# Kernel optimization log

Hardware: AMD Instinct MI355X
Metric: run time of the kernel (lower is better)

Reference implementation:

```python
import jax, jax.numpy as jnp
import numpy as np


def setup_inputs() -> dict:
    key = jax.random.key(0)
    ks = jax.random.split(key, 8)
    B, N, K, C_in, M, C_add, C_out = 2, 40000, 16, 64, 16, 3, 128
    in_features = (C_in + C_add) * M  # 1072
    input_features = jax.random.normal(ks[0], (B, N, C_in), dtype=jnp.float32)
    neighbor_inds = jax.random.randint(ks[1], (B, N, K), 0, N, dtype=jnp.int64)
    inverse_neighbors = jax.random.randint(ks[2], (B, N * K), 0, N * K, dtype=jnp.int64)
    inverse_k = jax.random.randint(ks[3], (B, N * K), 0, K, dtype=jnp.int64)
    inverse_idx = jax.random.randint(ks[4], (B, N * K), 0, N, dtype=jnp.int64)
    weightnet = jax.random.normal(ks[5], (B, N, K, M), dtype=jnp.float32)
    additional_features = jax.random.normal(ks[6], (B, N, K, C_add), dtype=jnp.float32)
    bound = 1.0 / np.sqrt(in_features)
    kw, kb = jax.random.split(ks[7])
    linear_weight = jax.random.uniform(kw, (C_out, in_features), dtype=jnp.float32, minval=-bound, maxval=bound)
    linear_bias = jax.random.uniform(kb, (C_out,), dtype=jnp.float32, minval=-bound, maxval=bound)
    return {
        "input_features": input_features,
        "neighbor_inds": neighbor_inds,
        "inverse_neighbors": inverse_neighbors,
        "inverse_k": inverse_k,
        "inverse_idx": inverse_idx,
        "weightnet": weightnet,
        "additional_features": additional_features,
        "linear_weight": linear_weight,
        "linear_bias": linear_bias,
    }


def reference(input_features, neighbor_inds, inverse_neighbors, inverse_k, inverse_idx,
              weightnet, additional_features, linear_weight, linear_bias):
    # inverse_* tensors are only used by the custom CUDA backward; unused here.
    B, N, K = neighbor_inds.shape
    # gather neighbor features: [B, N, K, C_in]
    gathered = jnp.take_along_axis(input_features[:, :, None, :],
                                   neighbor_inds[..., None], axis=1)
    # concat extra per-neighbor features -> [B, N, K, C]
    feats = jnp.concatenate([gathered, additional_features], axis=-1)
    # PConv: [B,N,C,K] @ [B,N,K,M] -> [B,N,C,M] -> flatten to [B,N,C*M]
    pconv = jnp.einsum('bnkc,bnkm->bncm', feats, weightnet)
    pconv = pconv.reshape(B, N, -1)
    # fused linear
    out = jnp.einsum('bnf,of->bno', pconv, linear_weight) + linear_bias
    return out
```

## Files before the change

### kernel.cpp

```cpp
#include <hip/hip_runtime.h>
#include <hip/hip_bf16.h>
#include <stdint.h>

typedef unsigned short u16;
typedef short short8 __attribute__((ext_vector_type(8)));
typedef float floatx4 __attribute__((ext_vector_type(4)));

#define NPERB   40000
#define NPTS    80000
#define KNBR    16
#define CIN     64
#define MDIM    16
#define CADD    3
#define CF      (CIN + CADD)
#define COUT    128
#define KF      1072
#define KP      1088

__device__ __forceinline__ u16 f2bf(float f) {
    union { float f; unsigned int u; } v; v.f = f;
    unsigned int u = v.u;
    return (u16)((u + 0x7FFFu + ((u >> 16) & 1u)) >> 16);
}
__device__ __forceinline__ short8 pack8(floatx4 x, floatx4 y) {
    union { short8 v; u16 a[8]; } u;
    u.a[0] = f2bf(x[0]); u.a[1] = f2bf(x[1]); u.a[2] = f2bf(x[2]); u.a[3] = f2bf(x[3]);
    u.a[4] = f2bf(y[0]); u.a[5] = f2bf(y[1]); u.a[6] = f2bf(y[2]); u.a[7] = f2bf(y[3]);
    return u.v;
}

__global__ void prep_lw_kernel(const float* __restrict__ lw, u16* __restrict__ lwp) {
    int i = blockIdx.x * 256 + threadIdx.x;
    if (i >= COUT * KP) return;
    int o = i / KP, f = i - o * KP;
    lwp[i] = (f < KF) ? f2bf(lw[(size_t)o * KF + f]) : (u16)0;
}

__global__ __launch_bounds__(256) void stage1_kernel(
    const float* __restrict__ inp,
    const int*   __restrict__ nbr,
    const float* __restrict__ wn,
    const float* __restrict__ addl,
    u16* __restrict__ pc,
    int chunk_start, int count)
{
    __shared__ __align__(16) float wsm[4][KNBR * MDIM];
    const int wave = threadIdx.x >> 6;
    const int lane = threadIdx.x & 63;
    const int lp = blockIdx.x * 4 + wave;
    const int p = chunk_start + lp;
    const int b = p / NPERB;

    {
        const floatx4* wn4 = (const floatx4*)(wn + (size_t)p * (KNBR * MDIM));
        ((floatx4*)&wsm[wave][0])[lane] = wn4[lane];
    }
    __syncthreads();

    const floatx4* wrow = (const floatx4*)&wsm[wave][0];
    const float* inpb = inp + (size_t)b * NPERB * CIN;
    const int* nbrp = nbr + (size_t)p * KNBR;

    floatx4 a0 = 0, a1 = 0, a2 = 0, a3 = 0;
#pragma unroll
    for (int k = 0; k < KNBR; k++) {
        int idx = nbrp[k];
        float fv = inpb[(size_t)idx * CIN + lane];
        a0 += fv * wrow[k * 4 + 0];
        a1 += fv * wrow[k * 4 + 1];
        a2 += fv * wrow[k * 4 + 2];
        a3 += fv * wrow[k * 4 + 3];
    }

    u16* row = pc + (size_t)lp * KP;
    *(short8*)(row + lane * 16)     = pack8(a0, a1);
    *(short8*)(row + lane * 16 + 8) = pack8(a2, a3);

    if (lane < CADD) {
        const float* ap = addl + (size_t)p * (KNBR * CADD) + lane;
        floatx4 c0 = 0, c1 = 0, c2 = 0, c3 = 0;
#pragma unroll
        for (int k = 0; k < KNBR; k++) {
            float av = ap[(size_t)k * CADD];
            c0 += av * wrow[k * 4 + 0];
            c1 += av * wrow[k * 4 + 1];
            c2 += av * wrow[k * 4 + 2];
            c3 += av * wrow[k * 4 + 3];
        }
        u16* r2 = row + CIN * MDIM + lane * 16;
        *(short8*)(r2)     = pack8(c0, c1);
        *(short8*)(r2 + 8) = pack8(c2, c3);
    } else if (lane == CADD) {
        short8 z = {0,0,0,0,0,0,0,0};
        *(short8*)(row + KF)     = z;
        *(short8*)(row + KF + 8) = z;
    }
}

__global__ __launch_bounds__(256) void stage2_kernel(
    const u16*   __restrict__ pc,
    const u16*   __restrict__ lwp,
    const float* __restrict__ bias,
    float* __restrict__ out,
    int chunk_start, int count)
{
    const int wave = threadIdx.x >> 6;
    const int lane = threadIdx.x & 63;
    const int r16  = lane & 15;
    const int quad = lane >> 4;
    const int r0 = blockIdx.x * 128 + (wave >> 1) * 64;
    const int c0 = (wave & 1) * 64;

    const u16* Abase = pc  + (size_t)(r0 + r16) * KP + quad * 8;
    const u16* Bbase = lwp + (size_t)(c0 + r16) * KP + quad * 8;

    floatx4 acc[4][4];
#pragma unroll
    for (int i = 0; i < 4; i++)
#pragma unroll
        for (int j = 0; j < 4; j++) acc[i][j] = 0;

#pragma unroll 2
    for (int kt = 0; kt < KP / 32; kt++) {
        short8 a[4], b[4];
#pragma unroll
        for (int i = 0; i < 4; i++)
            a[i] = *(const short8*)(Abase + (size_t)i * 16 * KP + kt * 32);
#pragma unroll
        for (int j = 0; j < 4; j++)
            b[j] = *(const short8*)(Bbase + (size_t)j * 16 * KP + kt * 32);
#pragma unroll
        for (int i = 0; i < 4; i++)
#pragma unroll
            for (int j = 0; j < 4; j++)
                acc[i][j] = __builtin_amdgcn_mfma_f32_16x16x32_bf16(
                    a[i], b[j], acc[i][j], 0, 0, 0);
    }

    const int p0 = chunk_start + r0;
#pragma unroll
    for (int j = 0; j < 4; j++) {
        int col = c0 + j * 16 + r16;
        float bv = bias[col];
#pragma unroll
        for (int i = 0; i < 4; i++) {
#pragma unroll
            for (int r = 0; r < 4; r++) {
                int prow = p0 + i * 16 + quad * 4 + r;
                out[(size_t)prow * COUT + col] = acc[i][j][r] + bv;
            }
        }
    }
}

__global__ __launch_bounds__(256) void fused_fallback_kernel(
    const float* __restrict__ inp, const int* __restrict__ nbr,
    const float* __restrict__ wn, const float* __restrict__ addl,
    const float* __restrict__ lw, const float* __restrict__ bias,
    float* __restrict__ out)
{
    const int p = blockIdx.x;
    const int b = p / NPERB;
    const int tid = threadIdx.x;
    __shared__ float sf[KNBR * CF];
    __shared__ float sw[KNBR * MDIM];
    __shared__ float sp[KF];

    sw[tid] = wn[(size_t)p * (KNBR * MDIM) + tid];
    for (int i = tid; i < KNBR * CIN; i += 256) {
        int k = i >> 6, c = i & 63;
        int idx = nbr[(size_t)p * KNBR + k];
        sf[k * CF + c] = inp[((size_t)b * NPERB + idx) * CIN + c];
    }
    if (tid < KNBR * CADD) {
        int k = tid / CADD, c = tid - k * CADD;
        sf[k * CF + CIN + c] = addl[(size_t)p * (KNBR * CADD) + tid];
    }
    __syncthreads();
    for (int f = tid; f < KF; f += 256) {
        int c = f >> 4, m = f & 15;
        float s = 0;
#pragma unroll
        for (int k = 0; k < KNBR; k++) s += sf[k * CF + c] * sw[k * MDIM + m];
        sp[f] = s;
    }
    __syncthreads();
    const int o = tid >> 1, h = tid & 1;
    float s = 0;
    for (int f = h * (KF / 2); f < (h + 1) * (KF / 2); f++)
        s += sp[f] * lw[(size_t)o * KF + f];
    s += __shfl_xor(s, 1);
    if (h == 0) out[(size_t)p * COUT + o] = s + bias[o];
}

extern "C" void kernel_launch(void* const* d_in, const int* in_sizes, int n_in,
                              void* d_out, int out_size, void* d_ws, size_t ws_size,
                              hipStream_t stream) {
    const float* inp  = (const float*)d_in[0];
    const int*   nbr  = (const int*)d_in[1];
    const float* wn   = (const float*)d_in[5];
    const float* addl = (const float*)d_in[6];
    const float* lw   = (const float*)d_in[7];
    const float* bias = (const float*)d_in[8];
    float* out = (float*)d_out;

    const size_t lw_bytes = (size_t)COUT * KP * sizeof(u16);
    const size_t row_bytes = (size_t)KP * sizeof(u16);

    size_t need_min = lw_bytes + 128 * row_bytes;
    if (ws_size < need_min) {
        fused_fallback_kernel<<<NPTS, 256, 0, stream>>>(inp, nbr, wn, addl, lw, bias, out);
        return;
    }

    u16* lwp = (u16*)d_ws;
    u16* pc  = (u16*)((char*)d_ws + lw_bytes);

    size_t avail = ws_size - lw_bytes;
    long long maxc = (long long)(avail / row_bytes);
    maxc = (maxc / 128) * 128;
    int chunk = (maxc >= NPTS) ? NPTS : (int)maxc;

    prep_lw_kernel<<<(COUT * KP + 255) / 256, 256, 0, stream>>>(lw, lwp);
    for (int start = 0; start < NPTS; start += chunk) {
        int count = NPTS - start;
        if (count > chunk) count = chunk;
        stage1_kernel<<<count / 4, 256, 0, stream>>>(inp, nbr, wn, addl, pc, start, count);
        stage2_kernel<<<count / 128, 256, 0, stream>>>(pc, lwp, bias, out, start, count);
    }
}
```

Before: 357.6 us.

## Fuse gather-PConv and linear GEMM into one kernel via LDS tile

Merges the two stages into a single kernel. Each block computes the bf16 PConv rows for 16 points into shared memory, laid out in k-tile slabs, and then runs the MFMA GEMM against the pre-converted linear weights. This removes the global round trip of the ~170 MB intermediate pc buffer and one launch. The cost is a much smaller GEMM tile per block (16 rows), so each block rereads all of the B weights, which raises L2 traffic. The additional-features product is also redistributed across lanes with shuffles.

After: 391.3 us. 1.09x slower.

```diff
diff --git a/kernel.cpp b/kernel.cpp
--- a/kernel.cpp
+++ b/kernel.cpp
@@ -1,5 +1,4 @@
 #include <hip/hip_runtime.h>
-#include <hip/hip_bf16.h>
 #include <stdint.h>
 
 typedef unsigned short u16;
@@ -16,6 +15,9 @@
 #define COUT    128
 #define KF      1072
 #define KP      1088
+#define NKT     34
+#define SLAB    65
+#define PTSB    16
 
 __device__ __forceinline__ u16 f2bf(float f) {
     union { float f; unsigned int u; } v; v.f = f;
@@ -36,120 +38,90 @@
     lwp[i] = (f < KF) ? f2bf(lw[(size_t)o * KF + f]) : (u16)0;
 }
 
-__global__ __launch_bounds__(256) void stage1_kernel(
+__global__ __launch_bounds__(256) void fused_kernel(
     const float* __restrict__ inp,
     const int*   __restrict__ nbr,
     const float* __restrict__ wn,
     const float* __restrict__ addl,
-    u16* __restrict__ pc,
-    int chunk_start, int count)
+    const u16*   __restrict__ lwp,
+    const float* __restrict__ bias,
+    float* __restrict__ out)
 {
+    __shared__ __align__(16) u16   Apc[NKT * SLAB * 8];
     __shared__ __align__(16) float wsm[4][KNBR * MDIM];
+
     const int wave = threadIdx.x >> 6;
     const int lane = threadIdx.x & 63;
-    const int lp = blockIdx.x * 4 + wave;
-    const int p = chunk_start + lp;
-    const int b = p / NPERB;
+    const int pbase = blockIdx.x * PTSB;
+    const float* inpb = inp + ((pbase >= NPERB) ? (size_t)NPERB * CIN : 0);
 
-    {
-        const floatx4* wn4 = (const floatx4*)(wn + (size_t)p * (KNBR * MDIM));
-        ((floatx4*)&wsm[wave][0])[lane] = wn4[lane];
+    for (int i = 0; i < PTSB / 4; i++) {
+        const int pr = wave * 4 + i;
+        const int p  = pbase + pr;
+
+        floatx4 w4 = ((const floatx4*)(wn + (size_t)p * (KNBR * MDIM)))[lane];
+        *(floatx4*)&wsm[wave][lane * 4] = w4;
+
+        float av_hold = (lane < KNBR * CADD)
+                          ? addl[(size_t)p * (KNBR * CADD) + lane] : 0.f;
+
+        const int* nbrp = nbr + (size_t)p * KNBR;
+        const floatx4* wrow = (const floatx4*)&wsm[wave][0];
+
+        floatx4 a0 = 0, a1 = 0, a2 = 0, a3 = 0;
+#pragma unroll
+        for (int k = 0; k < KNBR; k++) {
+            int idx = nbrp[k];
+            float fv = inpb[(size_t)idx * CIN + lane];
+            a0 += fv * wrow[k * 4 + 0];
+            a1 += fv * wrow[k * 4 + 1];
+            a2 += fv * wrow[k * 4 + 2];
+            a3 += fv * wrow[k * 4 + 3];
+        }
+        {
+            const int kt = lane >> 1, qb = (lane & 1) * 2;
+            u16* ch = &Apc[(unsigned)(kt * SLAB + pr * 4 + qb) * 8];
+            *(short8*)ch       = pack8(a0, a1);
+            *(short8*)(ch + 8) = pack8(a2, a3);
+        }
+
+        {
+            const int ec = lane >> 4, em = lane & 15;
+            float ev = 0.f;
+#pragma unroll
+            for (int k = 0; k < KNBR; k++) {
+                float av = __shfl(av_hold, k * CADD + ec);
+                ev += av * wsm[wave][k * MDIM + em];
+            }
+            if (ec == 3) ev = 0.f;
+            const int kt = 32 + (lane >> 5), quad = (lane >> 3) & 3;
+            Apc[(unsigned)(kt * SLAB + pr * 4 + quad) * 8 + (lane & 7)] = f2bf(ev);
+        }
     }
     __syncthreads();
 
-    const floatx4* wrow = (const floatx4*)&wsm[wave][0];
-    const float* inpb = inp + (size_t)b * NPERB * CIN;
-    const int* nbrp = nbr + (size_t)p * KNBR;
+    const int r16 = lane & 15, quad = lane >> 4;
+    const int c0 = wave * 32;
+    const u16* B0p = lwp + (size_t)(c0 + r16) * KP + quad * 8;
+    const u16* B1p = B0p + (size_t)16 * KP;
 
-    floatx4 a0 = 0, a1 = 0, a2 = 0, a3 = 0;
-#pragma unroll
-    for (int k = 0; k < KNBR; k++) {
-        int idx = nbrp[k];
-        float fv = inpb[(size_t)idx * CIN + lane];
-        a0 += fv * wrow[k * 4 + 0];
-        a1 += fv * wrow[k * 4 + 1];
-        a2 += fv * wrow[k * 4 + 2];
-        a3 += fv * wrow[k * 4 + 3];
+    floatx4 acc0 = 0, acc1 = 0;
+#pragma unroll 2
+    for (int kt = 0; kt < NKT; kt++) {
+        short8 A  = *(const short8*)&Apc[(unsigned)(kt * SLAB + r16 * 4 + quad) * 8];
+        short8 B0 = *(const short8*)(B0p + kt * 32);
+        short8 B1 = *(const short8*)(B1p + kt * 32);
+        acc0 = __builtin_amdgcn_mfma_f32_16x16x32_bf16(A, B0, acc0, 0, 0, 0);
+        acc1 = __builtin_amdgcn_mfma_f32_16x16x32_bf16(A, B1, acc1, 0, 0, 0);
     }
 
-    u16* row = pc + (size_t)lp * KP;
-    *(short8*)(row + lane * 16)     = pack8(a0, a1);
-    *(short8*)(row + lane * 16 + 8) = pack8(a2, a3);
-
-    if (lane < CADD) {
-        const float* ap = addl + (size_t)p * (KNBR * CADD) + lane;
-        floatx4 c0 = 0, c1 = 0, c2 = 0, c3 = 0;
+    const float bv0 = bias[c0 + r16];
+    const float bv1 = bias[c0 + 16 + r16];
 #pragma unroll
-        for (int k = 0; k < KNBR; k++) {
-            float av = ap[(size_t)k * CADD];
-            c0 += av * wrow[k * 4 + 0];
-            c1 += av * wrow[k * 4 + 1];
-            c2 += av * wrow[k * 4 + 2];
-            c3 += av * wrow[k * 4 + 3];
-        }
-        u16* r2 = row + CIN * MDIM + lane * 16;
-        *(short8*)(r2)     = pack8(c0, c1);
-        *(short8*)(r2 + 8) = pack8(c2, c3);
-    } else if (lane == CADD) {
-        short8 z = {0,0,0,0,0,0,0,0};
-        *(short8*)(row + KF)     = z;
-        *(short8*)(row + KF + 8) = z;
-    }
-}
-
-__global__ __launch_bounds__(256) void stage2_kernel(
-    const u16*   __restrict__ pc,
-    const u16*   __restrict__ lwp,
-    const float* __restrict__ bias,
-    float* __restrict__ out,
-    int chunk_start, int count)
-{
-    const int wave = threadIdx.x >> 6;
-    const int lane = threadIdx.x & 63;
-    const int r16  = lane & 15;
-    const int quad = lane >> 4;
-    const int r0 = blockIdx.x * 128 + (wave >> 1) * 64;
-    const int c0 = (wave & 1) * 64;
-
-    const u16* Abase = pc  + (size_t)(r0 + r16) * KP + quad * 8;
-    const u16* Bbase = lwp + (size_t)(c0 + r16) * KP + quad * 8;
-
-    floatx4 acc[4][4];
-#pragma unroll
-    for (int i = 0; i < 4; i++)
-#pragma unroll
-        for (int j = 0; j < 4; j++) acc[i][j] = 0;
-
-#pragma unroll 2
-    for (int kt = 0; kt < KP / 32; kt++) {
-        short8 a[4], b[4];
-#pragma unroll
-        for (int i = 0; i < 4; i++)
-            a[i] = *(const short8*)(Abase + (size_t)i * 16 * KP + kt * 32);
-#pragma unroll
-        for (int j = 0; j < 4; j++)
-            b[j] = *(const short8*)(Bbase + (size_t)j * 16 * KP + kt * 32);
-#pragma unroll
-        for (int i = 0; i < 4; i++)
-#pragma unroll
-            for (int j = 0; j < 4; j++)
-                acc[i][j] = __builtin_amdgcn_mfma_f32_16x16x32_bf16(
-                    a[i], b[j], acc[i][j], 0, 0, 0);
-    }
-
-    const int p0 = chunk_start + r0;
-#pragma unroll
-    for (int j = 0; j < 4; j++) {
-        int col = c0 + j * 16 + r16;
-        float bv = bias[col];
-#pragma unroll
-        for (int i = 0; i < 4; i++) {
-#pragma unroll
-            for (int r = 0; r < 4; r++) {
-                int prow = p0 + i * 16 + quad * 4 + r;
-                out[(size_t)prow * COUT + col] = acc[i][j][r] + bv;
-            }
-        }
+    for (int r = 0; r < 4; r++) {
+        const size_t row = (size_t)(pbase + quad * 4 + r) * COUT;
+        out[row + c0 + r16]      = acc0[r] + bv0;
+        out[row + c0 + 16 + r16] = acc1[r] + bv1;
     }
 }
 
@@ -205,27 +177,11 @@
     float* out = (float*)d_out;
 
     const size_t lw_bytes = (size_t)COUT * KP * sizeof(u16);
-    const size_t row_bytes = (size_t)KP * sizeof(u16);
-
-    size_t need_min = lw_bytes + 128 * row_bytes;
-    if (ws_size < need_min) {
+    if (ws_size < lw_bytes) {
         fused_fallback_kernel<<<NPTS, 256, 0, stream>>>(inp, nbr, wn, addl, lw, bias, out);
         return;
     }
-
     u16* lwp = (u16*)d_ws;
-    u16* pc  = (u16*)((char*)d_ws + lw_bytes);
-
-    size_t avail = ws_size - lw_bytes;
-    long long maxc = (long long)(avail / row_bytes);
-    maxc = (maxc / 128) * 128;
-    int chunk = (maxc >= NPTS) ? NPTS : (int)maxc;
-
     prep_lw_kernel<<<(COUT * KP + 255) / 256, 256, 0, stream>>>(lw, lwp);
-    for (int start = 0; start < NPTS; start += chunk) {
-        int count = NPTS - start;
-        if (count > chunk) count = chunk;
-        stage1_kernel<<<count / 4, 256, 0, stream>>>(inp, nbr, wn, addl, pc, start, count);
-        stage2_kernel<<<count / 128, 256, 0, stream>>>(pc, lwp, bias, out, start, count);
-    }
+    fused_kernel<<<NPTS / PTSB, 256, 0, stream>>>(inp, nbr, wn, addl, lwp, bias, out);
 }
```
